# Kernel tuning notes

Measured on AMD Instinct MI355X. Metric: run time of the kernel, lower is better.

## Reference

```python
import jax, jax.numpy as jnp
import numpy as np

C = 256
SCALE = 2
K = 3
GROUPS = 4


def _conv(x, w, b=None, groups=1, pad=0):
    y = jax.lax.conv_general_dilated(
        x, w, window_strides=(1, 1), padding=[(pad, pad), (pad, pad)],
        dimension_numbers=("NCHW", "OIHW", "NCHW"), feature_group_count=groups)
    if b is not None:
        y = y + b[None, :, None, None]
    return y


def _bn(x, g, b, m, v):
    # eval-mode BatchNorm2d, eps=1e-5
    scale = g / jnp.sqrt(v + 1e-5)
    return (x - m[None, :, None, None]) * scale[None, :, None, None] + b[None, :, None, None]


def _silu(x):
    return x * jax.nn.sigmoid(x)


def setup_inputs() -> dict:
    key = jax.random.key(0)
    ks = jax.random.split(key, 16)
    c = C
    s2k2 = SCALE ** 2 * K ** 2
    p = lambda k, shape, sc=0.05: jax.random.normal(k, shape, dtype=jnp.float32) * sc
    return {
        "x": jax.random.normal(ks[0], (8, c, 64, 64), dtype=jnp.float32),
        # kernel_compressor: 1x1, c -> c//2
        "Wkc": p(ks[1], (c // 2, c, 1, 1)), "bkc": p(ks[2], (c // 2,)),
        # kernel_predictor: 3x3 c//2 -> c//4, BN, SiLU, 1x1 -> s^2*k^2
        "Wkp1": p(ks[3], (c // 4, c // 2, 3, 3)), "bkp1": p(ks[4], (c // 4,)),
        "g1": 1.0 + p(ks[5], (c // 4,)), "be1": p(ks[6], (c // 4,)),
        "m1": p(ks[7], (c // 4,)), "v1": 1.0 + jax.random.uniform(ks[8], (c // 4,), dtype=jnp.float32),
        "Wkp2": p(ks[9], (s2k2, c // 4, 1, 1)), "bkp2": p(ks[10], (s2k2,)),
        # grouped 3x3 "deform" conv: c -> c, groups=4, no bias
        "Wdef": p(ks[11], (c, c // GROUPS, 3, 3)),
        # semantic gate
        "Wg1": p(ks[12], (c // 4, c, 1, 1)), "bg1": p(ks[13], (c // 4,)),
        "Wg2": p(ks[14], (c, c // 4, 1, 1)), "bg2": p(ks[15], (c,)),
    }


def reference(x, Wkc, bkc, Wkp1, bkp1, g1, be1, m1, v1, Wkp2, bkp2, Wdef, Wg1, bg1, Wg2, bg2):
    b, c, h, w = x.shape
    s, k = SCALE, K
    # --- dynamic reassembly kernel prediction ---
    comp = _conv(x, Wkc, bkc)                                    # (b, c/2, h, w)
    t = _silu(_bn(_conv(comp, Wkp1, bkp1, pad=1), g1, be1, m1, v1))
    kw = _conv(t, Wkp2, bkp2)                                    # (b, s^2*k^2, h, w)
    kw = kw.transpose(0, 2, 3, 1).reshape(b, h, w, s * s, k * k)
    kw = jax.nn.softmax(kw, axis=-1)
    # --- unfold (k x k patches, pad k//2), F.unfold ordering: kernel pos i*k+j ---
    xp = jnp.pad(x, ((0, 0), (0, 0), (1, 1), (1, 1)))
    patches = jnp.stack([xp[:, :, i:i + h, j:j + w]
                         for i in range(k) for j in range(k)], axis=-1)  # (b,c,h,w,k^2)
    kernel_out = jnp.einsum('bchwk,bhwsk->bhwsc', patches, kw)           # (b,h,w,s^2,c)
    kernel_out = kernel_out.transpose(0, 4, 1, 3, 2).reshape(b, c, h * s, w * s)
    # --- grouped conv branch + bilinear upsample (align_corners=False) ---
    enh = _conv(x, Wdef, None, groups=GROUPS, pad=1)
    up = jax.image.resize(enh, (b, c, h * s, w * s), method='linear')
    fused = kernel_out + up
    # --- SE-style semantic gate ---
    pooled = jnp.mean(fused, axis=(2, 3), keepdims=True)
    gate = jax.nn.sigmoid(_conv(_silu(_conv(pooled, Wg1, bg1)), Wg2, bg2))
    return fused * gate
```

## Files before the change

### kernel.cpp

```cpp
#include <hip/hip_runtime.h>
#include <hip/hip_bf16.h>

typedef __hip_bfloat16 bf16;
typedef __attribute__((ext_vector_type(8))) short short8;
typedef __attribute__((ext_vector_type(4))) float floatx4;

__device__ __forceinline__ float cvt(float v){ return v; }
__device__ __forceinline__ float cvt(bf16 v){ return __bfloat162float(v); }
__device__ __forceinline__ unsigned short f2bu(float f){
    union { float f; unsigned u; } uf; uf.f = f;
    unsigned u = uf.u;
    return (unsigned short)((u + 0x7FFFu + ((u>>16)&1u)) >> 16);
}
__device__ __forceinline__ float bu2f(unsigned short b){
    union { unsigned u; float f; } uf; uf.u = ((unsigned)b)<<16; return uf.f;
}
__device__ __forceinline__ floatx4 mfma16(short8 a, short8 b, floatx4 c){
    return __builtin_amdgcn_mfma_f32_16x16x32_bf16(a, b, c, 0, 0, 0);
}
__device__ __forceinline__ int swz8(int row, int part){
    return row*32 + ((part ^ ((row>>1)&3))<<3);
}
template<typename T>
__device__ __forceinline__ void ld4(const T* p, float& o0, float& o1, float& o2, float& o3){
    T t[4]; __builtin_memcpy(t, p, 4*sizeof(T));
    o0=cvt(t[0]); o1=cvt(t[1]); o2=cvt(t[2]); o3=cvt(t[3]);
}
__device__ __forceinline__ void ld2f(const float* p, float& o0, float& o1){
    float t[2]; __builtin_memcpy(t, p, 8);
    o0=t[0]; o1=t[1];
}

constexpr size_t O_KW    = 0;
constexpr size_t O_ENH   = O_KW    + 1179648;
constexpr size_t O_XBT   = O_ENH   + 8388608;
constexpr size_t O_COMPB = O_XBT   + 4194304;
constexpr size_t O_TB    = O_COMPB + 2097152;
constexpr size_t O_POOL  = O_TB    + 1048576;
constexpr size_t O_GATE  = O_POOL  + 2048;
constexpr size_t O_WKC   = O_GATE  + 2048;
constexpr size_t O_BKC   = O_WKC   + 32768;
constexpr size_t O_WKP1  = O_BKC   + 128;
constexpr size_t O_ALPHA = O_WKP1  + 73728;
constexpr size_t O_BETA  = O_ALPHA + 64;
constexpr size_t O_WKP2  = O_BETA  + 64;
constexpr size_t O_BKP2  = O_WKP2  + 2304;
constexpr size_t O_WDEF  = O_BKP2  + 64;
constexpr size_t O_WG1   = O_WDEF  + 147456;
constexpr size_t O_BG1   = O_WG1   + 16384;
constexpr size_t O_WG2   = O_BG1   + 64;
constexpr size_t O_BG2   = O_WG2   + 16384;
constexpr size_t O_FLAG  = O_BG2   + 256;
constexpr size_t O_WKCB  = (O_FLAG + 1 + 3) & ~(size_t)3;
constexpr size_t O_WKP1B = O_WKCB  + 16384;
constexpr size_t O_WDEFB = O_WKP1B + 36864;

__global__ __launch_bounds__(256) void kdet(const unsigned* __restrict__ w, float* flag)
{
    int hits = 0;
    for (int i = threadIdx.x; i < 16384; i += 256){
        unsigned v = w[i];
        hits += (((v >> 7) & 0xFFu) == 0xFFu) ? 1 : 0;
    }
    __shared__ int sh[256];
    sh[threadIdx.x] = hits;
    __syncthreads();
    for (int o = 128; o > 0; o >>= 1){
        if (threadIdx.x < o) sh[threadIdx.x] += sh[threadIdx.x + o];
        __syncthreads();
    }
    if (threadIdx.x == 0) flag[0] = (sh[0] > 0) ? 1.0f : 0.0f;
}

template<typename T>
__device__ __forceinline__ void k0_body(
    const T* Wkc, const T* bkc, const T* Wkp1, const T* bkp1,
    const T* g1, const T* be1, const T* m1, const T* v1,
    const T* Wkp2, const T* bkp2, const T* Wdef,
    const T* Wg1, const T* bg1, const T* Wg2, const T* bg2,
    float* ws)
{
    int i = blockIdx.x*256 + threadIdx.x;
    if (i < 32768){ ws[O_WKC+i] = cvt(Wkc[i]); return; }  i -= 32768;
    if (i < 128)  { ws[O_BKC+i] = cvt(bkc[i]); return; }  i -= 128;
    if (i < 73728){ ws[O_WKP1+i]= cvt(Wkp1[i]); return; } i -= 73728;
    if (i < 64){
        float a = cvt(g1[i]) / sqrtf(cvt(v1[i]) + 1e-5f);
        ws[O_ALPHA+i] = a;
        ws[O_BETA+i]  = (cvt(bkp1[i]) - cvt(m1[i]))*a + cvt(be1[i]);
        return;
    } i -= 64;
    if (i < 2304) { ws[O_WKP2+i] = cvt(Wkp2[i]); return; } i -= 2304;
    if (i < 36)   { ws[O_BKP2+i] = cvt(bkp2[i]); return; } i -= 36;
    if (i < 147456){ ws[O_WDEF+i]= cvt(Wdef[i]); return; } i -= 147456;
    if (i < 16384){ ws[O_WG1+i]  = cvt(Wg1[i]); return; }  i -= 16384;
    if (i < 64)   { ws[O_BG1+i]  = cvt(bg1[i]); return; }  i -= 64;
    if (i < 16384){ ws[O_WG2+i]  = cvt(Wg2[i]); return; }  i -= 16384;
    if (i < 256)  { ws[O_BG2+i]  = cvt(bg2[i]); return; }  i -= 256;
    if (i < 2048) { ws[O_POOL+i] = 0.f; return; }
}

__global__ __launch_bounds__(256) void k0_prep(
    const void* Wkc, const void* bkc, const void* Wkp1, const void* bkp1,
    const void* g1, const void* be1, const void* m1, const void* v1,
    const void* Wkp2, const void* bkp2, const void* Wdef,
    const void* Wg1, const void* bg1, const void* Wg2, const void* bg2,
    float* ws)
{
    if (ws[O_FLAG] > 0.5f)
        k0_body<float>((const float*)Wkc,(const float*)bkc,(const float*)Wkp1,(const float*)bkp1,
                       (const float*)g1,(const float*)be1,(const float*)m1,(const float*)v1,
                       (const float*)Wkp2,(const float*)bkp2,(const float*)Wdef,
                       (const float*)Wg1,(const float*)bg1,(const float*)Wg2,(const float*)bg2, ws);
    else
        k0_body<bf16>((const bf16*)Wkc,(const bf16*)bkc,(const bf16*)Wkp1,(const bf16*)bkp1,
                      (const bf16*)g1,(const bf16*)be1,(const bf16*)m1,(const bf16*)v1,
                      (const bf16*)Wkp2,(const bf16*)bkp2,(const bf16*)Wdef,
                      (const bf16*)Wg1,(const bf16*)bg1,(const bf16*)Wg2,(const bf16*)bg2, ws);
}

__global__ __launch_bounds__(256) void k0b_pack(float* ws)
{
    unsigned short* wkcb  = (unsigned short*)(ws + O_WKCB);
    unsigned short* wkp1b = (unsigned short*)(ws + O_WKP1B);
    unsigned short* wdefb = (unsigned short*)(ws + O_WDEFB);
    int i = blockIdx.x*256 + threadIdx.x;
    if (i < 32768){
        int kc = i>>12, cout = (i>>5)&127, cil = i&31;
        wkcb[i] = f2bu(ws[O_WKC + (size_t)cout*256 + kc*32 + cil]);
        return;
    } i -= 32768;
    if (i < 73728){
        int ch = i/18432, r = i - ch*18432;
        int kp = r>>11, cout = (r>>5)&63, cil = r&31;
        wkp1b[i] = f2bu(ws[O_WKP1 + ((size_t)cout*128 + ch*32 + cil)*9 + kp]);
        return;
    } i -= 73728;
    if (i < 147456){
        int g = i/36864, r1 = i - g*36864;
        int ch = r1/18432, r2 = r1 - ch*18432;
        int kp = r2>>11, cout = (r2>>5)&63, cil = r2&31;
        wdefb[i] = f2bu(ws[O_WDEF + (((size_t)(g*64+cout))*64 + ch*32 + cil)*9 + kp]);
    }
}

template<typename T>
__device__ __forceinline__ void xcvt_body(const T* __restrict__ x, unsigned short* __restrict__ xbt,
                                          float* lT)
{
    const int b = blockIdx.y;
    const int ci0 = (blockIdx.x & 3) * 64;
    const int pos0 = (blockIdx.x >> 2) * 64;
    const int lane = threadIdx.x & 63;
    const int wrow = threadIdx.x >> 6;
    for (int i = wrow; i < 64; i += 4)
        lT[i*65 + lane] = cvt(x[((size_t)(b*256 + ci0 + i))*4096 + pos0 + lane]);
    __syncthreads();
    for (int u = threadIdx.x; u < 2048; u += 256){
        const int pr = u >> 5, pc = u & 31;
        unsigned lo = f2bu(lT[(2*pc)*65 + pr]);
        unsigned hi = f2bu(lT[(2*pc+1)*65 + pr]);
        *(unsigned*)&xbt[((size_t)(b*4096) + pos0 + pr)*256 + ci0 + 2*pc] = lo | (hi<<16);
    }
}

__global__ __launch_bounds__(256) void xcvt(const void* x, unsigned short* xbt, const float* flag)
{
    __shared__ float lT[64*65];
    if (*flag > 0.5f) xcvt_body<float>((const float*)x, xbt, lT);
    else              xcvt_body<bf16>((const bf16*)x, xbt, lT);
}

__global__ __launch_bounds__(256) void k1_mfma(
    const unsigned short* __restrict__ xbt, const unsigned short* __restrict__ wb,
    const float* __restrict__ bias, unsigned short* __restrict__ compb)
{
    __shared__ __align__(16) short lA[128*32];
    __shared__ __align__(16) short lB[128*32];
    const int b = blockIdx.y, pos0 = blockIdx.x*128;
    const int tid = threadIdx.x;
    const int wave = tid>>6, lane = tid&63, q = lane>>4, r16 = lane&15;
    const int mh = (wave&1)*64, nh = (wave>>1)*64;
    floatx4 zero = {0.f,0.f,0.f,0.f};
    floatx4 acc[4][4];
    #pragma unroll
    for (int m=0;m<4;m++){ acc[m][0]=zero; acc[m][1]=zero; acc[m][2]=zero; acc[m][3]=zero; }

    for (int kc=0;kc<8;kc++){
        __syncthreads();
        {
            const short8* s = (const short8*)(wb + kc*4096);
            const int u0 = tid, u1 = tid + 256;
            *(short8*)&lA[swz8(u0>>2, u0&3)] = s[u0];
            *(short8*)&lA[swz8(u1>>2, u1&3)] = s[u1];
        }
        {
            #pragma unroll
            for (int k=0;k<2;k++){
                const int u = tid + k*256;
                const int p = u>>2, part = u&3;
                *(short8*)&lB[swz8(p, part)] =
                    *(const short8*)(xbt + ((size_t)(b*4096)+pos0+p)*256 + kc*32 + part*8);
            }
        }
        __syncthreads();
        short8 af[4], bfr[4];
        #pragma unroll
        for (int mt=0;mt<4;mt++) af[mt]  = *(const short8*)&lA[swz8(mh + mt*16 + r16, q)];
        #pragma unroll
        for (int nt=0;nt<4;nt++) bfr[nt] = *(const short8*)&lB[swz8(nh + nt*16 + r16, q)];
        #pragma unroll
        for (int mt=0;mt<4;mt++)
            #pragma unroll
            for (int nt=0;nt<4;nt++)
                acc[mt][nt] = mfma16(af[mt], bfr[nt], acc[mt][nt]);
    }
    #pragma unroll
    for (int mt=0;mt<4;mt++){
        const int cb = mh + mt*16 + q*4;
        const float b0=bias[cb], b1=bias[cb+1], b2=bias[cb+2], b3=bias[cb+3];
        #pragma unroll
        for (int nt=0;nt<4;nt++){
            const int pos = pos0 + nh + nt*16 + r16;
            floatx4 v = acc[mt][nt];
            uint2 pk;
            pk.x = (unsigned)f2bu(v.x+b0) | ((unsigned)f2bu(v.y+b1)<<16);
            pk.y = (unsigned)f2bu(v.z+b2) | ((unsigned)f2bu(v.w+b3)<<16);
            *(uint2*)(compb + ((size_t)(b*4096)+pos)*128 + cb) = pk;
        }
    }
}

__global__ __launch_bounds__(256) void conv3x3_all(
    const unsigned short* __restrict__ xbt, const unsigned short* __restrict__ compb,
    const unsigned short* __restrict__ wkp1b, const unsigned short* __restrict__ wdefb,
    const float* __restrict__ alpha, const float* __restrict__ beta,
    unsigned short* __restrict__ tb, float* __restrict__ enh)
{
    __shared__ __align__(16) short lX[6*66*32];
    __shared__ __align__(16) short lW[9*64*32];
    const int row0 = blockIdx.x*4, b = blockIdx.y, z = blockIdx.z;
    const bool isKP = (z == 0);
    const int g = isKP ? 0 : (z-1);
    const int CICH  = isKP ? 4 : 2;
    const int CITOT = isKP ? 128 : 256;
    const int cibase = g*64;
    const unsigned short* src  = isKP ? compb : xbt;
    const unsigned short* wsrc = isKP ? wkp1b : (wdefb + (size_t)g*36864);
    const int tid = threadIdx.x;
    const int wave = tid>>6, lane = tid&63, q = lane>>4, r16 = lane&15;
    floatx4 zero = {0.f,0.f,0.f,0.f};
    floatx4 acc[4][4];
    #pragma unroll
    for (int m=0;m<4;m++){ acc[m][0]=zero; acc[m][1]=zero; acc[m][2]=zero; acc[m][3]=zero; }

    {
        short8 zz = {0,0,0,0,0,0,0,0};
        short8* d = (short8*)lX;
        for (int i = tid; i < 1584; i += 256) d[i] = zz;
    }

    for (int ch = 0; ch < CICH; ch++){
        __syncthreads();
        {
            const short8* s = (const short8*)(wsrc + ch*18432);
            #pragma unroll
            for (int i=0;i<9;i++){
                const int u = tid + i*256;
                *(short8*)&lW[swz8(u>>2, u&3)] = s[u];
            }
        }
        {
            const int gc = tid>>2, part = tid&3;
            #pragma unroll
            for (int r=0;r<6;r++){
                const int gr = row0 - 1 + r;
                if ((unsigned)gr < 64u){
                    const unsigned short* sp = src +
                        ((size_t)(b*4096) + gr*64 + gc)*CITOT + cibase + ch*32 + part*8;
                    *(short8*)&lX[swz8(r*66 + 1 + gc, part)] = *(const short8*)sp;
                }
            }
        }
        __syncthreads();
        #pragma unroll
        for (int kp=0; kp<9; kp++){
            const int dr = kp/3, dc = kp - dr*3;
            short8 af[4], bfr[4];
            #pragma unroll
            for (int mt=0;mt<4;mt++)
                af[mt] = *(const short8*)&lW[swz8(kp*64 + mt*16 + r16, q)];
            #pragma unroll
            for (int nt=0;nt<4;nt++)
                bfr[nt] = *(const short8*)&lX[swz8((wave+dr)*66 + nt*16 + r16 + dc, q)];
            #pragma unroll
            for (int mt=0;mt<4;mt++)
                #pragma unroll
                for (int nt=0;nt<4;nt++)
                    acc[mt][nt] = mfma16(af[mt], bfr[nt], acc[mt][nt]);
        }
    }
    const int orow = row0 + wave;
    if (isKP){
        #pragma unroll
        for (int mt=0;mt<4;mt++){
            const int cb = mt*16 + q*4;
            const float a0=alpha[cb],a1=alpha[cb+1],a2=alpha[cb+2],a3=alpha[cb+3];
            const float e0=beta[cb],e1=beta[cb+1],e2=beta[cb+2],e3=beta[cb+3];
            #pragma unroll
            for (int nt=0;nt<4;nt++){
                const int pos = orow*64 + nt*16 + r16;
                floatx4 v = acc[mt][nt];
                float z0=v.x*a0+e0, z1=v.y*a1+e1, z2=v.z*a2+e2, z3=v.w*a3+e3;
                z0 = z0/(1.f+expf(-z0)); z1 = z1/(1.f+expf(-z1));
                z2 = z2/(1.f+expf(-z2)); z3 = z3/(1.f+expf(-z3));
                uint2 pk;
                pk.x = (unsigned)f2bu(z0) | ((unsigned)f2bu(z1)<<16);
                pk.y = (unsigned)f2bu(z2) | ((unsigned)f2bu(z3)<<16);
                *(uint2*)(tb + ((size_t)(b*4096)+pos)*64 + cb) = pk;
            }
        }
    } else {
        #pragma unroll
        for (int mt=0;mt<4;mt++){
            #pragma unroll
            for (int nt=0;nt<4;nt++){
                const int pos = orow*64 + nt*16 + r16;
                floatx4 v = acc[mt][nt];
                float* op = enh + ((size_t)(b*256) + g*64 + mt*16 + q*4)*4096 + pos;
                op[0]=v.x; op[4096]=v.y; op[8192]=v.z; op[12288]=v.w;
            }
        }
    }
}

__global__ __launch_bounds__(128) void k3_kpred(
    const unsigned short* __restrict__ tb, const float* __restrict__ W,
    const float* __restrict__ bias, float* __restrict__ kw)
{
    __shared__ float wl[2304];
    __shared__ float bl[36];
    for (int i=threadIdx.x;i<2304;i+=128) wl[i]=W[i];
    if (threadIdx.x<36) bl[threadIdx.x]=bias[threadIdx.x];
    __syncthreads();
    const int gid = blockIdx.x*128 + threadIdx.x;
    const unsigned short* tp = tb + (size_t)gid*64;
    float acc[36];
    #pragma unroll
    for (int o=0;o<36;o++) acc[o]=bl[o];
    #pragma unroll
    for (int c8=0;c8<8;c8++){
        uint4 pk = *(const uint4*)(tp + c8*8);
        unsigned u[4] = {pk.x, pk.y, pk.z, pk.w};
        float f[8];
        #pragma unroll
        for (int j=0;j<4;j++){
            f[2*j]   = bu2f((unsigned short)(u[j]&0xFFFFu));
            f[2*j+1] = bu2f((unsigned short)(u[j]>>16));
        }
        #pragma unroll
        for (int jj=0;jj<8;jj++){
            const int ci = c8*8+jj;
            #pragma unroll
            for (int o=0;o<36;o++) acc[o] += f[jj]*wl[o*64+ci];
        }
    }
    float* op = kw + (size_t)gid*36;
    #pragma unroll
    for (int s=0;s<4;s++){
        float mx = acc[s*9];
        #pragma unroll
        for (int k=1;k<9;k++) mx = fmaxf(mx, acc[s*9+k]);
        float e[9]; float sum=0.f;
        #pragma unroll
        for (int k=0;k<9;k++){ e[k]=expf(acc[s*9+k]-mx); sum+=e[k]; }
        float inv = 1.f/sum;
        #pragma unroll
        for (int k=0;k<9;k++) op[s*9+k] = e[k]*inv;
    }
}

template<typename T>
__device__ __forceinline__ void k5_body(
    const T* __restrict__ x, const float* __restrict__ kw,
    const float* __restrict__ enh, float* __restrict__ out,
    float* __restrict__ pooled, float* kwl)
{
    const int hi = blockIdx.x & 63;
    const int b  = blockIdx.x >> 6;
    const int c0 = blockIdx.y * 64;
    for (int i=threadIdx.x;i<2304;i+=256){
        int wi = i/36, r = i - wi*36;
        kwl[wi*37+r] = kw[((size_t)(b*4096 + hi*64 + wi))*36 + r];
    }
    __syncthreads();
    const int lane = threadIdx.x & 63;
    const int wv   = threadIdx.x >> 6;
    const int a    = lane & 31;
    const int hsel = lane >> 5;

    float k0r[36], k1r[36];
    #pragma unroll
    for (int r=0;r<36;r++) k0r[r] = kwl[(2*a)*37+r];
    #pragma unroll
    for (int r=0;r<36;r++) k1r[r] = kwl[(2*a+1)*37+r];

    const bool vy0 = hi>0, vy2 = hi<63;
    const int rm = vy0? hi-1 : 0;
    const int rp = vy2? hi+1 : 63;
    const int y0 = hi*2;
    const bool e0 = (a==0), e31 = (a==31);
    const int xb = e0 ? 0 : (e31 ? 60 : (2*a-1));
    const int eAb = e0 ? 0 : a-1;
    const int eBb = 31 + a;
    const int eAr = a+1;
    const int eBr = e31 ? 63 : 33+a;

    for (int it=0; it<8; ++it){
        const int c = c0 + (wv<<1) + hsel + (it<<3);
        const T* xc = x + ((size_t)(b*256)+c)*4096 + hi*64 + xb;
        float g[3][4];
        ld4(xc, g[1][0], g[1][1], g[1][2], g[1][3]);
        if (vy0) ld4(xc-64, g[0][0], g[0][1], g[0][2], g[0][3]);
        else     { g[0][0]=0.f; g[0][1]=0.f; g[0][2]=0.f; g[0][3]=0.f; }
        if (vy2) ld4(xc+64, g[2][0], g[2][1], g[2][2], g[2][3]);
        else     { g[2][0]=0.f; g[2][1]=0.f; g[2][2]=0.f; g[2][3]=0.f; }
        float w0[3][4];
        #pragma unroll
        for (int i=0;i<3;i++){
            float g0=g[i][0], g1=g[i][1], g2=g[i][2], g3=g[i][3];
            w0[i][0] = e0 ? 0.f : (e31 ? g1 : g0);
            w0[i][1] = e0 ? g0  : (e31 ? g2 : g1);
            w0[i][2] = e0 ? g1  : (e31 ? g3 : g2);
            w0[i][3] = e0 ? g2  : (e31 ? 0.f : g3);
        }
        float ko[2][4];
        #pragma unroll
        for (int s=0;s<4;s++){
            float a0c = 0.f, a1c = 0.f;
            #pragma unroll
            for (int i=0;i<3;i++){
                a0c += w0[i][0]*k0r[s*9+3*i] + w0[i][1]*k0r[s*9+3*i+1] + w0[i][2]*k0r[s*9+3*i+2];
                a1c += w0[i][1]*k1r[s*9+3*i] + w0[i][2]*k1r[s*9+3*i+1] + w0[i][3]*k1r[s*9+3*i+2];
            }
            ko[0][s]=a0c; ko[1][s]=a1c;
        }
        const float* ec = enh + ((size_t)(b*256)+c)*4096;
        float hAe[3], hAo[3], hBe[3], hBo[3];
        const int rows[3] = {rm, hi, rp};
        #pragma unroll
        for (int i=0;i<3;i++){
            const float* er = ec + rows[i]*64;
            float fA0, fA1; ld2f(er + eAb, fA0, fA1);
            float vAl = fA0, vAc = e0 ? fA0 : fA1;
            float vAr = er[eAr];
            float fB0, fB1; ld2f(er + eBb, fB0, fB1);
            float vBr = er[eBr];
            hAe[i] = 0.25f*vAl + 0.75f*vAc;
            hAo[i] = 0.75f*vAc + 0.25f*vAr;
            hBe[i] = 0.25f*fB0 + 0.75f*fB1;
            hBo[i] = 0.75f*fB1 + 0.25f*vBr;
        }
        float uAe0 = 0.25f*hAe[0] + 0.75f*hAe[1], uAe1 = 0.75f*hAe[1] + 0.25f*hAe[2];
        float uAo0 = 0.25f*hAo[0] + 0.75f*hAo[1], uAo1 = 0.75f*hAo[1] + 0.25f*hAo[2];
        float uBe0 = 0.25f*hBe[0] + 0.75f*hBe[1], uBe1 = 0.75f*hBe[1] + 0.25f*hBe[2];
        float uBo0 = 0.25f*hBo[0] + 0.75f*hBo[1], uBo1 = 0.75f*hBo[1] + 0.25f*hBo[2];
        float o00 = ko[0][0]+uAe0, o01 = ko[1][0]+uAo0;
        float o02 = ko[0][1]+uBe0, o03 = ko[1][1]+uBo0;
        float o10 = ko[0][2]+uAe1, o11 = ko[1][2]+uAo1;
        float o12 = ko[0][3]+uBe1, o13 = ko[1][3]+uBo1;
        float* o = out + (((size_t)(b*256)+c)*128 + y0)*128;
        *(float2*)(o + 2*a)        = make_float2(o00, o01);
        *(float2*)(o + 64 + 2*a)   = make_float2(o02, o03);
        *(float2*)(o + 128 + 2*a)  = make_float2(o10, o11);
        *(float2*)(o + 192 + 2*a)  = make_float2(o12, o13);
        float ps = (o00+o01) + (o02+o03) + (o10+o11) + (o12+o13);
        ps += __shfl_down(ps,16,32); ps += __shfl_down(ps, 8,32);
        ps += __shfl_down(ps, 4,32); ps += __shfl_down(ps, 2,32);
        ps += __shfl_down(ps, 1,32);
        if (a==0) atomicAdd(&pooled[b*256 + c], ps);
    }
}

__global__ __launch_bounds__(256) void k5_fuse(
    const void* x, const float* kw, const float* enh, float* out,
    float* pooled, const float* flag)
{
    __shared__ float kwl[64*37];
    if (*flag > 0.5f) k5_body<float>((const float*)x, kw, enh, out, pooled, kwl);
    else              k5_body<bf16>((const bf16*)x, kw, enh, out, pooled, kwl);
}

__global__ __launch_bounds__(256) void k7_gate(
    const float* __restrict__ pooled,
    const float* __restrict__ Wg1, const float* __restrict__ bg1,
    const float* __restrict__ Wg2, const float* __restrict__ bg2,
    float* __restrict__ gate)
{
    const int b = blockIdx.x;
    __shared__ float pl[256];
    __shared__ float hid[64];
    pl[threadIdx.x] = pooled[b*256+threadIdx.x] * (1.f/16384.f);
    __syncthreads();
    if (threadIdx.x < 64){
        float a = bg1[threadIdx.x];
        const float* w = Wg1 + (size_t)threadIdx.x*256;
        for (int c=0;c<256;c++) a += w[c]*pl[c];
        hid[threadIdx.x] = a/(1.f+expf(-a));
    }
    __syncthreads();
    float a = bg2[threadIdx.x];
    const float* w = Wg2 + (size_t)threadIdx.x*64;
    for (int j=0;j<64;j++) a += w[j]*hid[j];
    gate[b*256+threadIdx.x] = 1.f/(1.f+expf(-a));
}

__global__ __launch_bounds__(256) void k8_scale(
    float* __restrict__ out, const float* __restrict__ gate)
{
    const size_t gid = (size_t)blockIdx.x*256 + threadIdx.x;
    const float g = gate[gid>>12];
    float4* p = (float4*)out;
    float4 v = p[gid];
    v.x*=g; v.y*=g; v.z*=g; v.w*=g;
    p[gid] = v;
}

extern "C" void kernel_launch(void* const* d_in, const int* in_sizes, int n_in,
                              void* d_out, int out_size, void* d_ws, size_t ws_size,
                              hipStream_t stream)
{
    float* ws = (float*)d_ws;
    float* out = (float*)d_out;
    unsigned short* xbt   = (unsigned short*)(ws + O_XBT);
    unsigned short* compb = (unsigned short*)(ws + O_COMPB);
    unsigned short* tb    = (unsigned short*)(ws + O_TB);
    unsigned short* wkcb  = (unsigned short*)(ws + O_WKCB);
    unsigned short* wkp1b = (unsigned short*)(ws + O_WKP1B);
    unsigned short* wdefb = (unsigned short*)(ws + O_WDEFB);

    kdet<<<1, 256, 0, stream>>>((const unsigned*)d_in[1], ws + O_FLAG);
    k0_prep<<<1140, 256, 0, stream>>>(d_in[1],d_in[2],d_in[3],d_in[4],d_in[5],d_in[6],d_in[7],d_in[8],
                                      d_in[9],d_in[10],d_in[11],d_in[12],d_in[13],d_in[14],d_in[15], ws);
    k0b_pack<<<992, 256, 0, stream>>>(ws);
    xcvt<<<dim3(256,8), 256, 0, stream>>>(d_in[0], xbt, ws+O_FLAG);
    k1_mfma<<<dim3(32,8), 256, 0, stream>>>(xbt, wkcb, ws+O_BKC, compb);
    conv3x3_all<<<dim3(16,8,5), 256, 0, stream>>>(xbt, compb, wkp1b, wdefb,
                                                  ws+O_ALPHA, ws+O_BETA, tb, ws+O_ENH);
    k3_kpred<<<256, 128, 0, stream>>>(tb, ws+O_WKP2, ws+O_BKP2, ws+O_KW);
    k5_fuse<<<dim3(512,4), 256, 0, stream>>>(d_in[0], ws+O_KW, ws+O_ENH, out, ws+O_POOL, ws+O_FLAG);
    k7_gate<<<8, 256, 0, stream>>>(ws+O_POOL, ws+O_WG1, ws+O_BG1, ws+O_WG2, ws+O_BG2, ws+O_GATE);
    k8_scale<<<32768, 256, 0, stream>>>(out, ws+O_GATE);
}
```

Measured before the change: 352.2 us.

## Fuse kernel-predictor 1x1 and softmax into 3x3 conv, retile k1, grid-stride scale

The 1x1 kernel-predictor projection and its softmax now run in the epilogue of the 3x3 conv kernel. The SiLU output tile stays in LDS instead of making a bf16 round trip through global memory and a separate launch. The conv3x3 weights are now read straight from global memory instead of being staged in LDS, freeing shared memory for the fused epilogue. Separately, k1 uses 64-position tiles with twice as many blocks, and the final gate-scale kernel becomes a grid-stride loop over 2048 blocks. The cost is more global weight traffic and a heavy 36-accumulator epilogue in the z=0 blocks.

```diff
diff --git a/kernel.cpp b/kernel.cpp
--- a/kernel.cpp
+++ b/kernel.cpp
@@ -176,15 +176,15 @@
     const float* __restrict__ bias, unsigned short* __restrict__ compb)
 {
     __shared__ __align__(16) short lA[128*32];
-    __shared__ __align__(16) short lB[128*32];
-    const int b = blockIdx.y, pos0 = blockIdx.x*128;
+    __shared__ __align__(16) short lB[64*32];
+    const int b = blockIdx.y, pos0 = blockIdx.x*64;
     const int tid = threadIdx.x;
     const int wave = tid>>6, lane = tid&63, q = lane>>4, r16 = lane&15;
-    const int mh = (wave&1)*64, nh = (wave>>1)*64;
+    const int mh = (wave&1)*64, nh = (wave>>1)*32;
     floatx4 zero = {0.f,0.f,0.f,0.f};
-    floatx4 acc[4][4];
+    floatx4 acc[4][2];
     #pragma unroll
-    for (int m=0;m<4;m++){ acc[m][0]=zero; acc[m][1]=zero; acc[m][2]=zero; acc[m][3]=zero; }
+    for (int m=0;m<4;m++){ acc[m][0]=zero; acc[m][1]=zero; }
 
     for (int kc=0;kc<8;kc++){
         __syncthreads();
@@ -195,24 +195,20 @@
             *(short8*)&lA[swz8(u1>>2, u1&3)] = s[u1];
         }
         {
-            #pragma unroll
-            for (int k=0;k<2;k++){
-                const int u = tid + k*256;
-                const int p = u>>2, part = u&3;
-                *(short8*)&lB[swz8(p, part)] =
-                    *(const short8*)(xbt + ((size_t)(b*4096)+pos0+p)*256 + kc*32 + part*8);
-            }
-        }
-        __syncthreads();
-        short8 af[4], bfr[4];
+            const int p = tid>>2, part = tid&3;
+            *(short8*)&lB[swz8(p, part)] =
+                *(const short8*)(xbt + ((size_t)(b*4096)+pos0+p)*256 + kc*32 + part*8);
+        }
+        __syncthreads();
+        short8 af[4], bfr[2];
         #pragma unroll
         for (int mt=0;mt<4;mt++) af[mt]  = *(const short8*)&lA[swz8(mh + mt*16 + r16, q)];
         #pragma unroll
-        for (int nt=0;nt<4;nt++) bfr[nt] = *(const short8*)&lB[swz8(nh + nt*16 + r16, q)];
+        for (int nt=0;nt<2;nt++) bfr[nt] = *(const short8*)&lB[swz8(nh + nt*16 + r16, q)];
         #pragma unroll
         for (int mt=0;mt<4;mt++)
             #pragma unroll
-            for (int nt=0;nt<4;nt++)
+            for (int nt=0;nt<2;nt++)
                 acc[mt][nt] = mfma16(af[mt], bfr[nt], acc[mt][nt]);
     }
     #pragma unroll
@@ -220,7 +216,7 @@
         const int cb = mh + mt*16 + q*4;
         const float b0=bias[cb], b1=bias[cb+1], b2=bias[cb+2], b3=bias[cb+3];
         #pragma unroll
-        for (int nt=0;nt<4;nt++){
+        for (int nt=0;nt<2;nt++){
             const int pos = pos0 + nh + nt*16 + r16;
             floatx4 v = acc[mt][nt];
             uint2 pk;
@@ -235,10 +231,11 @@
     const unsigned short* __restrict__ xbt, const unsigned short* __restrict__ compb,
     const unsigned short* __restrict__ wkp1b, const unsigned short* __restrict__ wdefb,
     const float* __restrict__ alpha, const float* __restrict__ beta,
-    unsigned short* __restrict__ tb, float* __restrict__ enh)
-{
-    __shared__ __align__(16) short lX[6*66*32];
-    __shared__ __align__(16) short lW[9*64*32];
+    const float* __restrict__ Wkp2, const float* __restrict__ bkp2,
+    float* __restrict__ kw, float* __restrict__ enh)
+{
+    __shared__ __align__(16) short lXT[18432];
+    __shared__ float wl[2340];
     const int row0 = blockIdx.x*4, b = blockIdx.y, z = blockIdx.z;
     const bool isKP = (z == 0);
     const int g = isKP ? 0 : (z-1);
@@ -256,20 +253,16 @@
 
     {
         short8 zz = {0,0,0,0,0,0,0,0};
-        short8* d = (short8*)lX;
+        short8* d = (short8*)lXT;
         for (int i = tid; i < 1584; i += 256) d[i] = zz;
     }
+    if (isKP){
+        for (int i = tid; i < 2340; i += 256)
+            wl[i] = (i < 2304) ? Wkp2[i] : bkp2[i-2304];
+    }
 
     for (int ch = 0; ch < CICH; ch++){
         __syncthreads();
-        {
-            const short8* s = (const short8*)(wsrc + ch*18432);
-            #pragma unroll
-            for (int i=0;i<9;i++){
-                const int u = tid + i*256;
-                *(short8*)&lW[swz8(u>>2, u&3)] = s[u];
-            }
-        }
         {
             const int gc = tid>>2, part = tid&3;
             #pragma unroll
@@ -278,21 +271,22 @@
                 if ((unsigned)gr < 64u){
                     const unsigned short* sp = src +
                         ((size_t)(b*4096) + gr*64 + gc)*CITOT + cibase + ch*32 + part*8;
-                    *(short8*)&lX[swz8(r*66 + 1 + gc, part)] = *(const short8*)sp;
+                    *(short8*)&lXT[swz8(r*66 + 1 + gc, part)] = *(const short8*)sp;
                 }
             }
         }
         __syncthreads();
+        const unsigned short* wch = wsrc + ch*18432;
         #pragma unroll
         for (int kp=0; kp<9; kp++){
             const int dr = kp/3, dc = kp - dr*3;
             short8 af[4], bfr[4];
             #pragma unroll
             for (int mt=0;mt<4;mt++)
-                af[mt] = *(const short8*)&lW[swz8(kp*64 + mt*16 + r16, q)];
+                af[mt] = *(const short8*)(wch + (kp*64 + mt*16 + r16)*32 + q*8);
             #pragma unroll
             for (int nt=0;nt<4;nt++)
-                bfr[nt] = *(const short8*)&lX[swz8((wave+dr)*66 + nt*16 + r16 + dc, q)];
+                bfr[nt] = *(const short8*)&lXT[swz8((wave+dr)*66 + nt*16 + r16 + dc, q)];
             #pragma unroll
             for (int mt=0;mt<4;mt++)
                 #pragma unroll
@@ -300,8 +294,8 @@
                     acc[mt][nt] = mfma16(af[mt], bfr[nt], acc[mt][nt]);
         }
     }
-    const int orow = row0 + wave;
     if (isKP){
+        __syncthreads();
         #pragma unroll
         for (int mt=0;mt<4;mt++){
             const int cb = mt*16 + q*4;
@@ -309,7 +303,7 @@
             const float e0=beta[cb],e1=beta[cb+1],e2=beta[cb+2],e3=beta[cb+3];
             #pragma unroll
             for (int nt=0;nt<4;nt++){
-                const int pos = orow*64 + nt*16 + r16;
+                const int pl = wave*64 + nt*16 + r16;
                 floatx4 v = acc[mt][nt];
                 float z0=v.x*a0+e0, z1=v.y*a1+e1, z2=v.z*a2+e2, z3=v.w*a3+e3;
                 z0 = z0/(1.f+expf(-z0)); z1 = z1/(1.f+expf(-z1));
@@ -317,10 +311,43 @@
                 uint2 pk;
                 pk.x = (unsigned)f2bu(z0) | ((unsigned)f2bu(z1)<<16);
                 pk.y = (unsigned)f2bu(z2) | ((unsigned)f2bu(z3)<<16);
-                *(uint2*)(tb + ((size_t)(b*4096)+pos)*64 + cb) = pk;
+                *(uint2*)&lXT[pl*72 + cb] = pk;
             }
         }
+        __syncthreads();
+        const unsigned short* tp = (const unsigned short*)&lXT[tid*72];
+        float acc36[36];
+        #pragma unroll
+        for (int o=0;o<36;o++) acc36[o] = wl[2304+o];
+        #pragma unroll
+        for (int c8=0;c8<8;c8++){
+            short8 v8 = *(const short8*)(tp + c8*8);
+            float f[8];
+            #pragma unroll
+            for (int j=0;j<8;j++) f[j] = bu2f((unsigned short)v8[j]);
+            #pragma unroll
+            for (int jj=0;jj<8;jj++){
+                const int ci = c8*8+jj;
+                #pragma unroll
+                for (int o=0;o<36;o++) acc36[o] += f[jj]*wl[o*64+ci];
+            }
+        }
+        const int gid = b*4096 + (row0 + (tid>>6))*64 + (tid&63);
+        float* op = kw + (size_t)gid*36;
+        #pragma unroll
+        for (int s=0;s<4;s++){
+            float mx = acc36[s*9];
+            #pragma unroll
+            for (int k=1;k<9;k++) mx = fmaxf(mx, acc36[s*9+k]);
+            float e[9]; float sum=0.f;
+            #pragma unroll
+            for (int k=0;k<9;k++){ e[k]=expf(acc36[s*9+k]-mx); sum+=e[k]; }
+            float inv = 1.f/sum;
+            #pragma unroll
+            for (int k=0;k<9;k++) op[s*9+k] = e[k]*inv;
+        }
     } else {
+        const int orow = row0 + wave;
         #pragma unroll
         for (int mt=0;mt<4;mt++){
             #pragma unroll
@@ -331,52 +358,6 @@
                 op[0]=v.x; op[4096]=v.y; op[8192]=v.z; op[12288]=v.w;
             }
         }
-    }
-}
-
-__global__ __launch_bounds__(128) void k3_kpred(
-    const unsigned short* __restrict__ tb, const float* __restrict__ W,
-    const float* __restrict__ bias, float* __restrict__ kw)
-{
-    __shared__ float wl[2304];
-    __shared__ float bl[36];
-    for (int i=threadIdx.x;i<2304;i+=128) wl[i]=W[i];
-    if (threadIdx.x<36) bl[threadIdx.x]=bias[threadIdx.x];
-    __syncthreads();
-    const int gid = blockIdx.x*128 + threadIdx.x;
-    const unsigned short* tp = tb + (size_t)gid*64;
-    float acc[36];
-    #pragma unroll
-    for (int o=0;o<36;o++) acc[o]=bl[o];
-    #pragma unroll
-    for (int c8=0;c8<8;c8++){
-        uint4 pk = *(const uint4*)(tp + c8*8);
-        unsigned u[4] = {pk.x, pk.y, pk.z, pk.w};
-        float f[8];
-        #pragma unroll
-        for (int j=0;j<4;j++){
-            f[2*j]   = bu2f((unsigned short)(u[j]&0xFFFFu));
-            f[2*j+1] = bu2f((unsigned short)(u[j]>>16));
-        }
-        #pragma unroll
-        for (int jj=0;jj<8;jj++){
-            const int ci = c8*8+jj;
-            #pragma unroll
-            for (int o=0;o<36;o++) acc[o] += f[jj]*wl[o*64+ci];
-        }
-    }
-    float* op = kw + (size_t)gid*36;
-    #pragma unroll
-    for (int s=0;s<4;s++){
-        float mx = acc[s*9];
-        #pragma unroll
-        for (int k=1;k<9;k++) mx = fmaxf(mx, acc[s*9+k]);
-        float e[9]; float sum=0.f;
-        #pragma unroll
-        for (int k=0;k<9;k++){ e[k]=expf(acc[s*9+k]-mx); sum+=e[k]; }
-        float inv = 1.f/sum;
-        #pragma unroll
-        for (int k=0;k<9;k++) op[s*9+k] = e[k]*inv;
     }
 }
 
@@ -518,12 +499,13 @@
 __global__ __launch_bounds__(256) void k8_scale(
     float* __restrict__ out, const float* __restrict__ gate)
 {
-    const size_t gid = (size_t)blockIdx.x*256 + threadIdx.x;
-    const float g = gate[gid>>12];
     float4* p = (float4*)out;
-    float4 v = p[gid];
-    v.x*=g; v.y*=g; v.z*=g; v.w*=g;
-    p[gid] = v;
+    for (size_t gid = (size_t)blockIdx.x*256 + threadIdx.x; gid < 8388608u; gid += 524288u){
+        const float g = gate[gid>>12];
+        float4 v = p[gid];
+        v.x*=g; v.y*=g; v.z*=g; v.w*=g;
+        p[gid] = v;
+    }
 }
 
 extern "C" void kernel_launch(void* const* d_in, const int* in_sizes, int n_in,
@@ -534,7 +516,6 @@
     float* out = (float*)d_out;
     unsigned short* xbt   = (unsigned short*)(ws + O_XBT);
     unsigned short* compb = (unsigned short*)(ws + O_COMPB);
-    unsigned short* tb    = (unsigned short*)(ws + O_TB);
     unsigned short* wkcb  = (unsigned short*)(ws + O_WKCB);
     unsigned short* wkp1b = (unsigned short*)(ws + O_WKP1B);
     unsigned short* wdefb = (unsigned short*)(ws + O_WDEFB);
@@ -544,11 +525,12 @@
                                       d_in[9],d_in[10],d_in[11],d_in[12],d_in[13],d_in[14],d_in[15], ws);
     k0b_pack<<<992, 256, 0, stream>>>(ws);
     xcvt<<<dim3(256,8), 256, 0, stream>>>(d_in[0], xbt, ws+O_FLAG);
-    k1_mfma<<<dim3(32,8), 256, 0, stream>>>(xbt, wkcb, ws+O_BKC, compb);
+    k1_mfma<<<dim3(64,8), 256, 0, stream>>>(xbt, wkcb, ws+O_BKC, compb);
     conv3x3_all<<<dim3(16,8,5), 256, 0, stream>>>(xbt, compb, wkp1b, wdefb,
-                                                  ws+O_ALPHA, ws+O_BETA, tb, ws+O_ENH);
-    k3_kpred<<<256, 128, 0, stream>>>(tb, ws+O_WKP2, ws+O_BKP2, ws+O_KW);
+                                                  ws+O_ALPHA, ws+O_BETA,
+                                                  ws+O_WKP2, ws+O_BKP2,
+                                                  ws+O_KW, ws+O_ENH);
     k5_fuse<<<dim3(512,4), 256, 0, stream>>>(d_in[0], ws+O_KW, ws+O_ENH, out, ws+O_POOL, ws+O_FLAG);
     k7_gate<<<8, 256, 0, stream>>>(ws+O_POOL, ws+O_WG1, ws+O_BG1, ws+O_WG2, ws+O_BG2, ws+O_GATE);
-    k8_scale<<<32768, 256, 0, stream>>>(out, ws+O_GATE);
-}
+    k8_scale<<<2048, 256, 0, stream>>>(out, ws+O_GATE);
+}
```

Result: slower. 397.3 us (+12.8%).
